# Performance work log

Measured on AMD Instinct MI355X. Metric: run time of the kernel, lower is better.

The kernel has to match this reference:

```python
import jax, jax.numpy as jnp
import numpy as np

EPS = 1e-5  # torch nn.LayerNorm default eps
N_SUBJECTS = 16


def _gelu(x):
    # torch nn.GELU default = exact erf formulation
    return jax.nn.gelu(x, approximate=False)


def setup_inputs() -> dict:
    key = jax.random.key(0)
    ks = jax.random.split(key, 8)
    B, D = 131072, 512
    x = jax.random.normal(ks[0], (B, D), dtype=jnp.float32)
    groups = jax.random.randint(ks[1], (B,), 0, N_SUBJECTS, dtype=jnp.int32)
    # LayerNorm affine params: rows 0..15 subject-specific, row 16 = default_norm
    gammas = jnp.ones((N_SUBJECTS + 1, D), dtype=jnp.float32)
    betas = jnp.zeros((N_SUBJECTS + 1, D), dtype=jnp.float32)
    # Domain classifier MLP (xavier-uniform weights, zero biases)
    def xavier(k, fan_in, fan_out):
        lim = np.sqrt(6.0 / (fan_in + fan_out)).astype(np.float32)
        return jax.random.uniform(k, (fan_in, fan_out), dtype=jnp.float32,
                                  minval=-lim, maxval=lim)
    W1 = xavier(ks[2], D, 256); b1 = jnp.zeros((256,), jnp.float32)
    W2 = xavier(ks[3], 256, 128); b2 = jnp.zeros((128,), jnp.float32)
    W3 = xavier(ks[4], 128, N_SUBJECTS); b3 = jnp.zeros((N_SUBJECTS,), jnp.float32)
    return {"x": x, "groups": groups, "gammas": gammas, "betas": betas,
            "W1": W1, "b1": b1, "W2": W2, "b2": b2, "W3": W3, "b3": b3}


def _subject_layernorm(x, groups, gammas, betas):
    # Fused per-row LayerNorm with per-subject affine params.
    # Out-of-range subject ids (>= N_SUBJECTS or < 0) use the default row (index N_SUBJECTS).
    valid = (groups >= 0) & (groups < N_SUBJECTS)
    idx = jnp.where(valid, groups, N_SUBJECTS)
    g = gammas[idx]  # (B, D)
    b = betas[idx]   # (B, D)
    mu = jnp.mean(x, axis=-1, keepdims=True)
    var = jnp.mean(jnp.square(x - mu), axis=-1, keepdims=True)  # biased, as torch LN
    xn = (x - mu) * jax.lax.rsqrt(var + EPS)
    return xn * g + b


def _domain_classifier(x, W1, b1, W2, b2, W3, b3):
    # Dropout is identity in eval mode
    h = _gelu(x @ W1 + b1)
    h = _gelu(h @ W2 + b2)
    return h @ W3 + b3


def reference(x, groups, gammas, betas, W1, b1, W2, b2, W3, b3):
    # gradient reversal is identity in forward
    domain_logits = _domain_classifier(x, W1, b1, W2, b2, W3, b3)
    normalized_x = _subject_layernorm(x, groups, gammas, betas)
    return (normalized_x, domain_logits)
```

## Files before the change

### kernel.cpp

```cpp
#include <hip/hip_runtime.h>
#include <hip/hip_bf16.h>
#include <stdint.h>

#define NSUB 16

typedef short  bf16x8 __attribute__((ext_vector_type(8)));
typedef float  f32x4  __attribute__((ext_vector_type(4)));
typedef unsigned int u32x4 __attribute__((ext_vector_type(4)));

__device__ __forceinline__ float gelu_exact(float x){
  return 0.5f * x * (1.0f + erff(x * 0.70710678118654752440f));
}

__device__ __forceinline__ float gelu_fast(float x){
  float xx = x * x;
  float m  = fmaf(0.044715f, xx, 1.0f);
  float a  = x * m * -2.3022084f;
  float e  = __builtin_amdgcn_exp2f(a);
  float r  = __builtin_amdgcn_rcpf(e + 1.0f);
  return x * r;
}

__device__ __forceinline__ unsigned short f2bf(float f){
  union { float f; uint32_t u; } v; v.f = f;
  uint32_t u = v.u;
  return (unsigned short)((u + 0x7FFFu + ((u >> 16) & 1u)) >> 16);
}

__device__ __forceinline__ unsigned int pk2(float lo, float hi){
  union { __hip_bfloat162 b; unsigned int u; } c;
  c.b = __float22bfloat162_rn(make_float2(lo, hi));
  return c.u;
}

__device__ __forceinline__ bf16x8 as_bf(u32x4 v){
  union { u32x4 u; bf16x8 b; } c; c.u = v; return c.b;
}

__global__ __launch_bounds__(256) void wconv_kernel(
    const float* __restrict__ W1, const float* __restrict__ W2, const float* __restrict__ W3,
    unsigned short* __restrict__ W1f, unsigned short* __restrict__ W2f, unsigned short* __restrict__ W3f){
  int t = blockIdx.x * 256 + threadIdx.x;
  if (t < 131072){
    int n = t >> 9, k = t & 511;
    int lane = ((k >> 3) & 3) * 16 + (n & 15);
    int idx = (((k >> 5) * 16 + (n >> 4)) * 64 + lane) * 8 + (k & 7);
    W1f[idx] = f2bf(W1[k*256 + n]);
  } else if (t < 163840){
    int i = t - 131072; int n = i >> 8, k = i & 255;
    int lane = ((k >> 3) & 3) * 16 + (n & 15);
    int idx = (((k >> 5) * 8 + (n >> 4)) * 64 + lane) * 8 + (k & 7);
    W2f[idx] = f2bf(W2[k*128 + n]);
  } else if (t < 165888){
    int i = t - 163840; int n = i >> 7, k = i & 127;
    int lane = ((k >> 3) & 3) * 16 + n;
    int idx = ((k >> 5) * 64 + lane) * 8 + (k & 7);
    W3f[idx] = f2bf(W3[k*16 + n]);
  }
}

__global__ __launch_bounds__(512, 4) void fused_kernel(
    const float* __restrict__ x, const int* __restrict__ groups,
    const float* __restrict__ gammas, const float* __restrict__ betas,
    const unsigned short* __restrict__ W1f, const float* __restrict__ b1,
    const unsigned short* __restrict__ W2f, const float* __restrict__ b2,
    const unsigned short* __restrict__ W3f, const float* __restrict__ b3,
    float* __restrict__ ln_out, float* __restrict__ out2){
  __shared__ __align__(16) uint8_t smem[65536];
  constexpr int OFF_H2 = 32768;

  const int tid  = threadIdx.x;
  const int stripe = blockIdx.x / 3;
  const int role   = blockIdx.x - 3*stripe;
  const int row0   = stripe * 64;

  if (role != 0){
    const int lrow0 = row0 + (role - 1) * 32;
    const int sr = tid >> 4;
    const int sc = tid & 15;
    const float* xg = x + (size_t)(lrow0 + sr)*512 + sc*8;
    f32x4 xr0[4], xr1[4];
    #pragma unroll
    for (int c = 0; c < 4; ++c){
      xr0[c] = *(const f32x4*)(xg + c*128);
      xr1[c] = *(const f32x4*)(xg + c*128 + 4);
    }
    float s = 0.f, q = 0.f;
    #pragma unroll
    for (int c = 0; c < 4; ++c){
      s += xr0[c].x + xr0[c].y + xr0[c].z + xr0[c].w
         + xr1[c].x + xr1[c].y + xr1[c].z + xr1[c].w;
      q += xr0[c].x*xr0[c].x + xr0[c].y*xr0[c].y + xr0[c].z*xr0[c].z + xr0[c].w*xr0[c].w
         + xr1[c].x*xr1[c].x + xr1[c].y*xr1[c].y + xr1[c].z*xr1[c].z + xr1[c].w*xr1[c].w;
    }
    s += __shfl_xor(s, 1); s += __shfl_xor(s, 2);
    s += __shfl_xor(s, 4); s += __shfl_xor(s, 8);
    q += __shfl_xor(q, 1); q += __shfl_xor(q, 2);
    q += __shfl_xor(q, 4); q += __shfl_xor(q, 8);
    float mu  = s * (1.0f/512.0f);
    float var = q * (1.0f/512.0f) - mu*mu;
    float rs  = rsqrtf(var + 1e-5f);
    float nmr = -mu * rs;
    int gi   = groups[lrow0 + sr];
    int gidx = ((unsigned)gi < (unsigned)NSUB) ? gi : NSUB;
    const float* gpr = gammas + (size_t)gidx*512 + sc*8;
    const float* bpr = betas  + (size_t)gidx*512 + sc*8;
    float* op = ln_out + (size_t)(lrow0 + sr)*512 + sc*8;
    #pragma unroll
    for (int c = 0; c < 4; ++c){
      f32x4 g0 = *(const f32x4*)(gpr + c*128);
      f32x4 g1 = *(const f32x4*)(gpr + c*128 + 4);
      f32x4 e0 = *(const f32x4*)(bpr + c*128);
      f32x4 e1 = *(const f32x4*)(bpr + c*128 + 4);
      f32x4 o0, o1;
      o0.x = fmaf(fmaf(xr0[c].x, rs, nmr), g0.x, e0.x);
      o0.y = fmaf(fmaf(xr0[c].y, rs, nmr), g0.y, e0.y);
      o0.z = fmaf(fmaf(xr0[c].z, rs, nmr), g0.z, e0.z);
      o0.w = fmaf(fmaf(xr0[c].w, rs, nmr), g0.w, e0.w);
      o1.x = fmaf(fmaf(xr1[c].x, rs, nmr), g1.x, e1.x);
      o1.y = fmaf(fmaf(xr1[c].y, rs, nmr), g1.y, e1.y);
      o1.z = fmaf(fmaf(xr1[c].z, rs, nmr), g1.z, e1.z);
      o1.w = fmaf(fmaf(xr1[c].w, rs, nmr), g1.w, e1.w);
      *(f32x4*)(op + c*128)     = o0;
      *(f32x4*)(op + c*128 + 4) = o1;
    }
    return;
  }

  const int wave = tid >> 6;
  const int lane = tid & 63;
  const int l15  = lane & 15;
  const int g4   = lane >> 4;

  {
    const int sr  = tid >> 3;
    const int sc  = tid & 7;
    const int wb  = (sc*16) ^ ((sr & 7) << 4);
    uint8_t* xrow = smem + sr*1024;
    const float* xg = x + (size_t)(row0 + sr)*512 + sc*8;
    #pragma unroll
    for (int t = 0; t < 8; ++t){
      f32x4 v0 = *(const f32x4*)(xg + t*64);
      f32x4 v1 = *(const f32x4*)(xg + t*64 + 4);
      u32x4 pw;
      pw.x = pk2(v0.x, v0.y); pw.y = pk2(v0.z, v0.w);
      pw.z = pk2(v1.x, v1.y); pw.w = pk2(v1.z, v1.w);
      *(u32x4*)(xrow + t*128 + wb) = pw;
    }
  }

  u32x4 braw[4][2];
  #pragma unroll
  for (int p = 0; p < 3; ++p)
    #pragma unroll
    for (int n = 0; n < 2; ++n)
      braw[p][n] = *(const u32x4*)(W1f + (size_t)(((p*16 + wave*2 + n)*64 + lane)*8));

  float b1v[2];
  #pragma unroll
  for (int n = 0; n < 2; ++n) b1v[n] = b1[wave*32 + n*16 + l15];
  float b2v = b2[wave*16 + l15];
  float b3v = b3[l15];

  int baseA[4][2];
  #pragma unroll
  for (int m = 0; m < 4; ++m){
    int row = m*16 + l15;
    int sw  = (row & 7) << 4;
    int bse = row*1024 + ((g4*16) ^ (sw & 0x30));
    int kx  = (row >> 2) & 1;
    baseA[m][0] = bse + ((0 ^ kx) << 6);
    baseA[m][1] = bse + ((1 ^ kx) << 6);
  }

  __syncthreads();

  f32x4 acc1[4][2] = {};
  #pragma unroll
  for (int g = 0; g < 16; ++g){
    if (g < 13){
      #pragma unroll
      for (int n = 0; n < 2; ++n)
        braw[(g+3)&3][n] = *(const u32x4*)(W1f + (size_t)((((g+3)*16 + wave*2 + n)*64 + lane)*8));
    }
    bf16x8 a[4];
    #pragma unroll
    for (int m = 0; m < 4; ++m)
      a[m] = *(const bf16x8*)(smem + baseA[m][g & 1] + (g >> 1)*128);
    #pragma unroll
    for (int m = 0; m < 4; ++m)
      #pragma unroll
      for (int n = 0; n < 2; ++n)
        acc1[m][n] = __builtin_amdgcn_mfma_f32_16x16x32_bf16(a[m], as_bf(braw[g & 3][n]), acc1[m][n], 0, 0, 0);
  }

  u32x4 b2raw[4];
  #pragma unroll
  for (int p = 0; p < 3; ++p)
    b2raw[p] = *(const u32x4*)(W2f + (size_t)(((p*8 + wave)*64 + lane)*8));

  __syncthreads();

  #pragma unroll
  for (int n = 0; n < 2; ++n){
    #pragma unroll
    for (int m = 0; m < 4; ++m){
      #pragma unroll
      for (int r = 0; r < 4; ++r){
        int row = m*16 + g4*4 + r;
        int col = wave*32 + n*16 + l15;
        float v = gelu_fast(acc1[m][n][r] + b1v[n]);
        *(unsigned short*)(smem + row*512 + ((col*2) ^ ((row & 7) << 4))) = f2bf(v);
      }
    }
  }
  __syncthreads();

  int baseH[4][2];
  #pragma unroll
  for (int m = 0; m < 4; ++m){
    int row = m*16 + l15;
    int sw  = (row & 7) << 4;
    int bse = row*512 + ((g4*16) ^ (sw & 0x30));
    int kx  = (row >> 2) & 1;
    baseH[m][0] = bse + ((0 ^ kx) << 6);
    baseH[m][1] = bse + ((1 ^ kx) << 6);
  }
  f32x4 acc2[4] = {};
  #pragma unroll
  for (int g = 0; g < 8; ++g){
    if (g < 5)
      b2raw[(g+3)&3] = *(const u32x4*)(W2f + (size_t)((((g+3)*8 + wave)*64 + lane)*8));
    bf16x8 a[4];
    #pragma unroll
    for (int m = 0; m < 4; ++m)
      a[m] = *(const bf16x8*)(smem + baseH[m][g & 1] + (g >> 1)*128);
    #pragma unroll
    for (int m = 0; m < 4; ++m)
      acc2[m] = __builtin_amdgcn_mfma_f32_16x16x32_bf16(a[m], as_bf(b2raw[g & 3]), acc2[m], 0, 0, 0);
  }

  u32x4 b3raw[4];
  #pragma unroll
  for (int ks = 0; ks < 4; ++ks)
    b3raw[ks] = *(const u32x4*)(W3f + (size_t)((ks*64 + lane)*8));

  #pragma unroll
  for (int m = 0; m < 4; ++m){
    #pragma unroll
    for (int r = 0; r < 4; ++r){
      int row = m*16 + g4*4 + r;
      int col = wave*16 + l15;
      float v = gelu_fast(acc2[m][r] + b2v);
      *(unsigned short*)(smem + OFF_H2 + row*256 + ((col*2) ^ ((row & 7) << 4))) = f2bf(v);
    }
  }
  __syncthreads();

  if (wave < 4){
    int baseG[2];
    {
      int row = wave*16 + l15;
      int sw  = (row & 7) << 4;
      int bse = OFF_H2 + row*256 + ((g4*16) ^ (sw & 0x30));
      int kx  = (row >> 2) & 1;
      baseG[0] = bse + ((0 ^ kx) << 6);
      baseG[1] = bse + ((1 ^ kx) << 6);
    }
    f32x4 acc3 = {};
    #pragma unroll
    for (int ks = 0; ks < 4; ++ks){
      bf16x8 a = *(const bf16x8*)(smem + baseG[ks & 1] + (ks >> 1)*128);
      acc3 = __builtin_amdgcn_mfma_f32_16x16x32_bf16(a, as_bf(b3raw[ks]), acc3, 0, 0, 0);
    }
    #pragma unroll
    for (int r = 0; r < 4; ++r){
      int grow = row0 + wave*16 + g4*4 + r;
      out2[(size_t)grow*16 + l15] = acc3[r] + b3v;
    }
  }
}

__global__ __launch_bounds__(256) void ln_kernel(
    const float* __restrict__ x, const int* __restrict__ groups,
    const float* __restrict__ gammas, const float* __restrict__ betas,
    float* __restrict__ out){
  int row  = blockIdx.x * 4 + (threadIdx.x >> 6);
  int lane = threadIdx.x & 63;
  const float4* xrp = (const float4*)(x + (size_t)row * 512);
  float4 a = xrp[lane];
  float4 b = xrp[lane + 64];
  float s = a.x + a.y + a.z + a.w + b.x + b.y + b.z + b.w;
  float q = a.x*a.x + a.y*a.y + a.z*a.z + a.w*a.w
          + b.x*b.x + b.y*b.y + b.z*b.z + b.w*b.w;
  #pragma unroll
  for (int o = 32; o > 0; o >>= 1){
    s += __shfl_xor(s, o);
    q += __shfl_xor(q, o);
  }
  float mu  = s * (1.0f/512.0f);
  float var = q * (1.0f/512.0f) - mu*mu;
  float rsq = rsqrtf(var + 1e-5f);
  int gi = groups[row];
  int idx = ((unsigned)gi < (unsigned)NSUB) ? gi : NSUB;
  const float4* gr = (const float4*)(gammas + (size_t)idx * 512);
  const float4* br = (const float4*)(betas  + (size_t)idx * 512);
  float4 g0 = gr[lane], g1 = gr[lane + 64];
  float4 e0 = br[lane], e1 = br[lane + 64];
  float4 o0, o1;
  o0.x = (a.x - mu)*rsq*g0.x + e0.x; o0.y = (a.y - mu)*rsq*g0.y + e0.y;
  o0.z = (a.z - mu)*rsq*g0.z + e0.z; o0.w = (a.w - mu)*rsq*g0.w + e0.w;
  o1.x = (b.x - mu)*rsq*g1.x + e1.x; o1.y = (b.y - mu)*rsq*g1.y + e1.y;
  o1.z = (b.z - mu)*rsq*g1.z + e1.z; o1.w = (b.w - mu)*rsq*g1.w + e1.w;
  float4* orow = (float4*)(out + (size_t)row * 512);
  orow[lane]      = o0;
  orow[lane + 64] = o1;
}

__global__ __launch_bounds__(256) void mlp_naive(
    const float* __restrict__ x,
    const float* __restrict__ W1, const float* __restrict__ b1,
    const float* __restrict__ W2, const float* __restrict__ b2,
    const float* __restrict__ W3, const float* __restrict__ b3,
    float* __restrict__ out2){
  __shared__ float xr[512];
  __shared__ float h1[256];
  __shared__ float h2[128];
  int row = blockIdx.x, t = threadIdx.x;
  xr[t]       = x[(size_t)row*512 + t];
  xr[t + 256] = x[(size_t)row*512 + t + 256];
  __syncthreads();
  {
    float s = 0.f;
    for (int k = 0; k < 512; ++k) s += xr[k] * W1[k*256 + t];
    h1[t] = gelu_exact(s + b1[t]);
  }
  __syncthreads();
  if (t < 128){
    float s = 0.f;
    for (int k = 0; k < 256; ++k) s += h1[k] * W2[k*128 + t];
    h2[t] = gelu_exact(s + b2[t]);
  }
  __syncthreads();
  if (t < 16){
    float s = 0.f;
    for (int k = 0; k < 128; ++k) s += h2[k] * W3[k*16 + t];
    out2[(size_t)row*16 + t] = s + b3[t];
  }
}

extern "C" void kernel_launch(void* const* d_in, const int* in_sizes, int n_in,
                              void* d_out, int out_size, void* d_ws, size_t ws_size,
                              hipStream_t stream){
  const float* x      = (const float*)d_in[0];
  const int*   groups = (const int*)d_in[1];
  const float* gammas = (const float*)d_in[2];
  const float* betas  = (const float*)d_in[3];
  const float* W1 = (const float*)d_in[4];
  const float* b1 = (const float*)d_in[5];
  const float* W2 = (const float*)d_in[6];
  const float* b2 = (const float*)d_in[7];
  const float* W3 = (const float*)d_in[8];
  const float* b3 = (const float*)d_in[9];
  float* out  = (float*)d_out;
  const int B = in_sizes[0] / 512;
  float* out2 = out + (size_t)B * 512;

  const int n_u16 = 131072 + 32768 + 2048;
  const size_t ws_need = (size_t)n_u16 * sizeof(unsigned short);
  if (ws_size >= ws_need){
    unsigned short* W1f = (unsigned short*)d_ws;
    unsigned short* W2f = W1f + 131072;
    unsigned short* W3f = W2f + 32768;
    wconv_kernel<<<(n_u16 + 255)/256, 256, 0, stream>>>(W1, W2, W3, W1f, W2f, W3f);
    fused_kernel<<<3*(B/64), 512, 0, stream>>>(x, groups, gammas, betas,
                                               W1f, b1, W2f, b2, W3f, b3, out, out2);
  } else {
    mlp_naive<<<B, 256, 0, stream>>>(x, W1, b1, W2, b2, W3, b3, out2);
    ln_kernel<<<B/4, 256, 0, stream>>>(x, groups, gammas, betas, out);
  }
}
```

Baseline: 156.8 us.

## Halve LDS by staging x in two K-halves and remap block-to-stripe order

```diff
diff --git a/kernel.cpp b/kernel.cpp
--- a/kernel.cpp
+++ b/kernel.cpp
@@ -66,13 +66,22 @@
     const unsigned short* __restrict__ W2f, const float* __restrict__ b2,
     const unsigned short* __restrict__ W3f, const float* __restrict__ b3,
     float* __restrict__ ln_out, float* __restrict__ out2){
-  __shared__ __align__(16) uint8_t smem[65536];
-  constexpr int OFF_H2 = 32768;
-
-  const int tid  = threadIdx.x;
-  const int stripe = blockIdx.x / 3;
-  const int role   = blockIdx.x - 3*stripe;
-  const int row0   = stripe * 64;
+  __shared__ __align__(16) uint8_t smem[32768];
+
+  const int tid = threadIdx.x;
+  int stripe, role;
+  {
+    int nb  = gridDim.x;
+    int bid = blockIdx.x;
+    int per = nb >> 3;
+    if (((nb & 7) == 0) && (per % 3 == 0)){
+      int g = (bid & 7) * per + (bid >> 3);
+      stripe = g / 3; role = g - 3*stripe;
+    } else {
+      stripe = bid / 3; role = bid - 3*stripe;
+    }
+  }
+  const int row0 = stripe * 64;
 
   if (role != 0){
     const int lrow0 = row0 + (role - 1) * 32;
@@ -132,66 +141,98 @@
   const int l15  = lane & 15;
   const int g4   = lane >> 4;
 
+  const int ssr  = tid >> 3;
+  const int ssc  = tid & 7;
+  const int sswz = (ssr & 7) << 4;
+  uint8_t* xsrow = smem + ssr*512;
+  const float* xg0 = x + (size_t)(row0 + ssr)*512 + ssc*32;
+
+  #pragma unroll
+  for (int c = 0; c < 4; ++c){
+    f32x4 v0 = *(const f32x4*)(xg0 + c*8);
+    f32x4 v1 = *(const f32x4*)(xg0 + c*8 + 4);
+    u32x4 pw;
+    pw.x = pk2(v0.x, v0.y); pw.y = pk2(v0.z, v0.w);
+    pw.z = pk2(v1.x, v1.y); pw.w = pk2(v1.z, v1.w);
+    *(u32x4*)(xsrow + ((ssc*64 + c*16) ^ sswz)) = pw;
+  }
+
+  u32x4 braw[4][2];
+  #pragma unroll
+  for (int p = 0; p < 3; ++p)
+    #pragma unroll
+    for (int n = 0; n < 2; ++n)
+      braw[p][n] = *(const u32x4*)(W1f + (size_t)(((p*16 + wave*2 + n)*64 + lane)*8));
+
+  float b1v[2];
+  #pragma unroll
+  for (int n = 0; n < 2; ++n) b1v[n] = b1[wave*32 + n*16 + l15];
+  float b2v = b2[wave*16 + l15];
+  float b3v = b3[l15];
+
+  int baseX[4][2];
+  #pragma unroll
+  for (int m = 0; m < 4; ++m){
+    int row = m*16 + l15;
+    int sw  = (row & 7) << 4;
+    int bse = row*512 + ((g4*16) ^ (sw & 0x30));
+    int kx  = (row >> 2) & 1;
+    baseX[m][0] = bse + ((0 ^ kx) << 6);
+    baseX[m][1] = bse + ((1 ^ kx) << 6);
+  }
+
+  __syncthreads();
+
+  f32x4 acc1[4][2] = {};
+  #pragma unroll
+  for (int g = 0; g < 8; ++g){
+    #pragma unroll
+    for (int n = 0; n < 2; ++n)
+      braw[(g+3)&3][n] = *(const u32x4*)(W1f + (size_t)((((g+3)*16 + wave*2 + n)*64 + lane)*8));
+    bf16x8 a[4];
+    #pragma unroll
+    for (int m = 0; m < 4; ++m)
+      a[m] = *(const bf16x8*)(smem + baseX[m][g & 1] + (g >> 1)*128);
+    #pragma unroll
+    for (int m = 0; m < 4; ++m)
+      #pragma unroll
+      for (int n = 0; n < 2; ++n)
+        acc1[m][n] = __builtin_amdgcn_mfma_f32_16x16x32_bf16(a[m], as_bf(braw[g & 3][n]), acc1[m][n], 0, 0, 0);
+  }
+
+  __syncthreads();
+
   {
-    const int sr  = tid >> 3;
-    const int sc  = tid & 7;
-    const int wb  = (sc*16) ^ ((sr & 7) << 4);
-    uint8_t* xrow = smem + sr*1024;
-    const float* xg = x + (size_t)(row0 + sr)*512 + sc*8;
-    #pragma unroll
-    for (int t = 0; t < 8; ++t){
-      f32x4 v0 = *(const f32x4*)(xg + t*64);
-      f32x4 v1 = *(const f32x4*)(xg + t*64 + 4);
+    const float* xg1 = xg0 + 256;
+    #pragma unroll
+    for (int c = 0; c < 4; ++c){
+      f32x4 v0 = *(const f32x4*)(xg1 + c*8);
+      f32x4 v1 = *(const f32x4*)(xg1 + c*8 + 4);
       u32x4 pw;
       pw.x = pk2(v0.x, v0.y); pw.y = pk2(v0.z, v0.w);
       pw.z = pk2(v1.x, v1.y); pw.w = pk2(v1.z, v1.w);
-      *(u32x4*)(xrow + t*128 + wb) = pw;
-    }
-  }
-
-  u32x4 braw[4][2];
-  #pragma unroll
-  for (int p = 0; p < 3; ++p)
-    #pragma unroll
-    for (int n = 0; n < 2; ++n)
-      braw[p][n] = *(const u32x4*)(W1f + (size_t)(((p*16 + wave*2 + n)*64 + lane)*8));
-
-  float b1v[2];
-  #pragma unroll
-  for (int n = 0; n < 2; ++n) b1v[n] = b1[wave*32 + n*16 + l15];
-  float b2v = b2[wave*16 + l15];
-  float b3v = b3[l15];
-
-  int baseA[4][2];
-  #pragma unroll
-  for (int m = 0; m < 4; ++m){
-    int row = m*16 + l15;
-    int sw  = (row & 7) << 4;
-    int bse = row*1024 + ((g4*16) ^ (sw & 0x30));
-    int kx  = (row >> 2) & 1;
-    baseA[m][0] = bse + ((0 ^ kx) << 6);
-    baseA[m][1] = bse + ((1 ^ kx) << 6);
-  }
-
-  __syncthreads();
-
-  f32x4 acc1[4][2] = {};
-  #pragma unroll
-  for (int g = 0; g < 16; ++g){
-    if (g < 13){
+      *(u32x4*)(xsrow + ((ssc*64 + c*16) ^ sswz)) = pw;
+    }
+  }
+  __syncthreads();
+
+  #pragma unroll
+  for (int g = 0; g < 8; ++g){
+    int gg = 8 + g;
+    if (gg < 13){
       #pragma unroll
       for (int n = 0; n < 2; ++n)
-        braw[(g+3)&3][n] = *(const u32x4*)(W1f + (size_t)((((g+3)*16 + wave*2 + n)*64 + lane)*8));
+        braw[(gg+3)&3][n] = *(const u32x4*)(W1f + (size_t)((((gg+3)*16 + wave*2 + n)*64 + lane)*8));
     }
     bf16x8 a[4];
     #pragma unroll
     for (int m = 0; m < 4; ++m)
-      a[m] = *(const bf16x8*)(smem + baseA[m][g & 1] + (g >> 1)*128);
+      a[m] = *(const bf16x8*)(smem + baseX[m][g & 1] + (g >> 1)*128);
     #pragma unroll
     for (int m = 0; m < 4; ++m)
       #pragma unroll
       for (int n = 0; n < 2; ++n)
-        acc1[m][n] = __builtin_amdgcn_mfma_f32_16x16x32_bf16(a[m], as_bf(braw[g & 3][n]), acc1[m][n], 0, 0, 0);
+        acc1[m][n] = __builtin_amdgcn_mfma_f32_16x16x32_bf16(a[m], as_bf(braw[gg & 3][n]), acc1[m][n], 0, 0, 0);
   }
 
   u32x4 b2raw[4];
@@ -216,16 +257,6 @@
   }
   __syncthreads();
 
-  int baseH[4][2];
-  #pragma unroll
-  for (int m = 0; m < 4; ++m){
-    int row = m*16 + l15;
-    int sw  = (row & 7) << 4;
-    int bse = row*512 + ((g4*16) ^ (sw & 0x30));
-    int kx  = (row >> 2) & 1;
-    baseH[m][0] = bse + ((0 ^ kx) << 6);
-    baseH[m][1] = bse + ((1 ^ kx) << 6);
-  }
   f32x4 acc2[4] = {};
   #pragma unroll
   for (int g = 0; g < 8; ++g){
@@ -234,7 +265,7 @@
     bf16x8 a[4];
     #pragma unroll
     for (int m = 0; m < 4; ++m)
-      a[m] = *(const bf16x8*)(smem + baseH[m][g & 1] + (g >> 1)*128);
+      a[m] = *(const bf16x8*)(smem + baseX[m][g & 1] + (g >> 1)*128);
     #pragma unroll
     for (int m = 0; m < 4; ++m)
       acc2[m] = __builtin_amdgcn_mfma_f32_16x16x32_bf16(a[m], as_bf(b2raw[g & 3]), acc2[m], 0, 0, 0);
@@ -244,6 +275,8 @@
   #pragma unroll
   for (int ks = 0; ks < 4; ++ks)
     b3raw[ks] = *(const u32x4*)(W3f + (size_t)((ks*64 + lane)*8));
+
+  __syncthreads();
 
   #pragma unroll
   for (int m = 0; m < 4; ++m){
@@ -252,7 +285,7 @@
       int row = m*16 + g4*4 + r;
       int col = wave*16 + l15;
       float v = gelu_fast(acc2[m][r] + b2v);
-      *(unsigned short*)(smem + OFF_H2 + row*256 + ((col*2) ^ ((row & 7) << 4))) = f2bf(v);
+      *(unsigned short*)(smem + row*256 + ((col*2) ^ ((row & 7) << 4))) = f2bf(v);
     }
   }
   __syncthreads();
@@ -262,7 +295,7 @@
     {
       int row = wave*16 + l15;
       int sw  = (row & 7) << 4;
-      int bse = OFF_H2 + row*256 + ((g4*16) ^ (sw & 0x30));
+      int bse = row*256 + ((g4*16) ^ (sw & 0x30));
       int kx  = (row >> 2) & 1;
       baseG[0] = bse + ((0 ^ kx) << 6);
       baseG[1] = bse + ((1 ^ kx) << 6);
@@ -368,7 +401,7 @@
 
   const int n_u16 = 131072 + 32768 + 2048;
   const size_t ws_need = (size_t)n_u16 * sizeof(unsigned short);
-  if (ws_size >= ws_need){
+  if (ws_size >= ws_need && (B % 64) == 0){
     unsigned short* W1f = (unsigned short*)d_ws;
     unsigned short* W2f = W1f + 131072;
     unsigned short* W3f = W2f + 32768;
```

New measurement: 185.3 us. +18.2%, slower.
